# Kernel tuning notes

Hardware: AMD Instinct MI355X
Metric: run time of the kernel (lower is better)

## Reference

```python
import jax, jax.numpy as jnp
import numpy as np

DIM, E, K, H = 1024, 8, 2, 4096

def setup_inputs() -> dict:
    key = jax.random.key(0)
    ks = jax.random.split(key, 5)
    s_in = 1.0 / np.sqrt(DIM)
    s_h = 1.0 / np.sqrt(H)
    return {
        "x": jax.random.normal(ks[0], (4, 2048, DIM), dtype=jnp.float32),
        "Wr": jax.random.normal(ks[1], (DIM, E), dtype=jnp.float32) * s_in,
        "W1": jax.random.normal(ks[2], (E, DIM, H), dtype=jnp.float32) * s_in,
        "b1": jnp.zeros((E, H), dtype=jnp.float32),
        "W2": jax.random.normal(ks[3], (E, H, DIM), dtype=jnp.float32) * s_h,
        "b2": jnp.zeros((E, DIM), dtype=jnp.float32),
    }

def reference(x, Wr, W1, b1, W2, b2):
    batch, seq, dim = x.shape
    x_flat = x.reshape(-1, dim)                      # [T, D]
    logits = x_flat @ Wr                             # [T, E]
    w, ind = jax.lax.top_k(logits, K)                # [T, K]
    w = jax.nn.softmax(w, axis=-1)
    # combine[t, e] = sum_i w[t, i] * (ind[t, i] == e)
    combine = jnp.einsum('tke,tk->te', jax.nn.one_hot(ind, E, dtype=x.dtype), w)  # [T, E]

    def body(acc, params):
        W1e, b1e, W2e, b2e, ce = params
        h = jax.nn.gelu(x_flat @ W1e + b1e, approximate=False)  # exact GELU (torch nn.GELU default)
        y = h @ W2e + b2e                                        # [T, D]
        return acc + ce[:, None] * y, None

    out0 = jnp.zeros_like(x_flat)
    out, _ = jax.lax.scan(body, out0, (W1, b1, W2, b2, combine.T))
    return out.reshape(batch, seq, dim)
```

## Files before the change

### kernel.cpp

```cpp
#include <hip/hip_runtime.h>
#include <hip/hip_bf16.h>

#define TDIM 1024
#define NEXP 8
#define NHID 4096

typedef __hip_bfloat16 bf16;
typedef __attribute__((ext_vector_type(8))) short bf16x8;
typedef __attribute__((ext_vector_type(8))) unsigned short u16x8;
typedef __attribute__((ext_vector_type(4))) float f32x4;

__device__ __forceinline__ void gload_lds16(void* lds, const void* g) {
  __builtin_amdgcn_global_load_lds(
      (const __attribute__((address_space(1))) unsigned int*)g,
      (__attribute__((address_space(3))) unsigned int*)lds, 16, 0, 0);
}

__device__ __forceinline__ unsigned short f2bf_bits(float f) {
  __hip_bfloat16 b = __float2bfloat16(f);
  unsigned short u;
  __builtin_memcpy(&u, &b, 2);
  return u;
}

__device__ __forceinline__ float bf2f(unsigned short u) {
  union { unsigned int i; float f; } c;
  c.i = ((unsigned int)u) << 16;
  return c.f;
}

__device__ __forceinline__ void cvt_quad(const float* __restrict__ src, bf16* __restrict__ dst,
                                         int gid, int ngShift, int rowLen) {
  const int kqg = gid >> ngShift;
  const int ng = gid & ((1 << ngShift) - 1);
  const float* s = src + ((size_t)kqg * 8) * rowLen + ng * 4;
  float4 v[8];
#pragma unroll
  for (int j = 0; j < 8; ++j) v[j] = *reinterpret_cast<const float4*>(s + (size_t)j * rowLen);
  u16x8 o[4];
#pragma unroll
  for (int c = 0; c < 4; ++c)
#pragma unroll
    for (int j = 0; j < 8; ++j) o[c][j] = f2bf_bits((&v[j].x)[c]);
  bf16* d = dst + ((size_t)kqg * rowLen + ng * 4) * 8;
#pragma unroll
  for (int c = 0; c < 4; ++c) *reinterpret_cast<u16x8*>(d + c * 8) = o[c];
}

__global__ __launch_bounds__(256) void prep_kernel(
    const float* __restrict__ W1, bf16* __restrict__ W1C, const float* __restrict__ x,
    bf16* __restrict__ xb, const float* __restrict__ Wr, int* __restrict__ idx,
    float* __restrict__ wtok, int* __restrict__ cnt, int T) {
  __shared__ float xs[4][1024];
  const int pb = blockIdx.x;
  const int tid = threadIdx.x;
  if (pb < 4096) {
    cvt_quad(W1, W1C, pb * 256 + tid, 10, 4096);
  } else {
    const int p = pb - 4096;
    const int wave = p * 4 + (tid >> 6);
    const int lane = tid & 63;
    if (wave >= T) return;
    float* xrow = xs[tid >> 6];
    const float4* xr4 = reinterpret_cast<const float4*>(x + (size_t)wave * TDIM);
    bf16* xbrow = xb + (size_t)wave * TDIM;
#pragma unroll
    for (int i = 0; i < TDIM / 256; ++i) {
      float4 xv = xr4[lane + i * 64];
      ushort4 o;
      o.x = f2bf_bits(xv.x);
      o.y = f2bf_bits(xv.y);
      o.z = f2bf_bits(xv.z);
      o.w = f2bf_bits(xv.w);
      *reinterpret_cast<ushort4*>(xbrow + (lane + i * 64) * 4) = o;
      *reinterpret_cast<float4*>(&xrow[(lane + i * 64) * 4]) = xv;
    }
    float acc[NEXP];
#pragma unroll
    for (int e = 0; e < NEXP; ++e) acc[e] = 0.f;
    const float4* wr4 = reinterpret_cast<const float4*>(Wr);
#pragma unroll
    for (int i = 0; i < TDIM / 64; ++i) {
      float xv = xrow[lane + i * 64];
      float4 wa = wr4[(lane + i * 64) * 2];
      float4 wb = wr4[(lane + i * 64) * 2 + 1];
      acc[0] += xv * wa.x;
      acc[1] += xv * wa.y;
      acc[2] += xv * wa.z;
      acc[3] += xv * wa.w;
      acc[4] += xv * wb.x;
      acc[5] += xv * wb.y;
      acc[6] += xv * wb.z;
      acc[7] += xv * wb.w;
    }
#pragma unroll
    for (int e = 0; e < NEXP; ++e) {
      float v = acc[e];
#pragma unroll
      for (int s = 32; s; s >>= 1) v += __shfl_xor(v, s);
      acc[e] = v;
    }
    if (lane == 0) {
      int e0 = 0;
      float l0 = acc[0];
      for (int e = 1; e < NEXP; ++e)
        if (acc[e] > l0) { l0 = acc[e]; e0 = e; }
      int e1 = -1;
      float l1 = -INFINITY;
      for (int e = 0; e < NEXP; ++e)
        if (e != e0 && acc[e] > l1) { l1 = acc[e]; e1 = e; }
      float z = __expf(l1 - l0);
      idx[wave * 2] = e0;
      idx[wave * 2 + 1] = e1;
      wtok[wave * 2] = 1.f / (1.f + z);
      wtok[wave * 2 + 1] = z / (1.f + z);
      atomicAdd(&cnt[e0], 1);
      atomicAdd(&cnt[e1], 1);
    }
  }
}

__global__ void scan_kernel(const int* __restrict__ cnt, int* __restrict__ offs) {
  if (threadIdx.x == 0 && blockIdx.x == 0) {
    int s = 0;
    for (int e = 0; e < NEXP; ++e) { offs[e] = s; s += cnt[e]; }
  }
}

__global__ void build_perm_kernel(const int* __restrict__ idx, const int* __restrict__ offs,
                                  int* __restrict__ fill, int* __restrict__ perm,
                                  int* __restrict__ islot, int T) {
  int t = blockIdx.x * blockDim.x + threadIdx.x;
  if (t >= T) return;
#pragma unroll
  for (int k = 0; k < 2; ++k) {
    int e = idx[t * 2 + k];
    int p = offs[e] + atomicAdd(&fill[e], 1);
    perm[p] = t;
    islot[t * 2 + k] = p;
  }
}

#define DSR(dst, va, IMM) \
  asm volatile("ds_read_b128 %0, %1 offset:%2" : "=&v"(dst) : "v"(va), "i"(IMM))

template <int KD, int ND, bool GATHER, bool GELU, bool CONV>
__global__ __launch_bounds__(512, 2) void moe_gemm8(
    const bf16* __restrict__ A, const bf16* __restrict__ BC, const float* __restrict__ bias,
    const int* __restrict__ perm, const int* __restrict__ cnt, const int* __restrict__ offs,
    bf16* __restrict__ Dst, int nm, int nn, const float* __restrict__ Wsrc,
    bf16* __restrict__ Wdst) {
  __shared__ short lds[65536];

  const int nwg = NEXP * nm * nn;
  const int bid = blockIdx.x;
  if (CONV && bid >= nwg) {
    const int gid = (bid - nwg) * 512 + threadIdx.x;
    cvt_quad(Wsrc, Wdst, gid, 8, 1024);
    return;
  }
  const int wg = (bid & 7) * (nwg >> 3) + (bid >> 3);
  const int e = wg / (nm * nn);
  const int rem = wg % (nm * nn);
  const int mb = rem / nn, nb = rem % nn;

  const int ce = cnt[e];
  const int m0 = mb * 256;
  if (m0 >= ce) return;
  const int base = offs[e];
  const int n0 = nb * 256;
  const int tid = threadIdx.x;
  const int lane = tid & 63;
  const int wid = tid >> 6;
  const int wm = wid >> 2, wn = wid & 3;
  const int lcol = lane & 15;

  const unsigned ldsb = (unsigned)(size_t)&lds[0];
  const int v4 = lane >> 4;
  const int j7 = lcol & 7;
  const unsigned bk0 = (unsigned)((v4 ^ j7) << 4);
  const unsigned bk1 = (unsigned)(((v4 + 4) ^ j7) << 4);
  const unsigned aBase = ldsb + (unsigned)((wm * 64 + lcol) * 128);
  const unsigned vaA00 = aBase + bk0, vaA01 = aBase + bk1;
  const unsigned vaA10 = aBase + 65536u + bk0, vaA11 = aBase + 65536u + bk1;
  const unsigned bBase = ldsb + 32768u + (unsigned)(v4 * 2048 + (wn * 32 + lcol) * 16);
  const unsigned vaB0 = bBase, vaB1 = bBase + 65536u;

  const bf16* aP[2][2];
  const bf16* bP[2][2];
#pragma unroll
  for (int h = 0; h < 2; ++h)
#pragma unroll
    for (int i = 0; i < 2; ++i) {
      int s = tid + i * 512;
      int srow = s >> 3;
      int ksrc = (s & 7) ^ (srow & 7);
      int grow = m0 + h * 128 + srow;
      if (grow > ce - 1) grow = ce - 1;
      size_t arow = GATHER ? (size_t)perm[base + grow] : (size_t)(base + grow);
      aP[h][i] = A + arow * KD + ksrc * 8;
      int jo = s >> 7, brow = s & 127;
      bP[h][i] = BC + (size_t)e * KD * ND + ((size_t)jo * ND + (n0 + h * 128 + brow)) * 8;
    }

  f32x4 acc[8][4];
#pragma unroll
  for (int m = 0; m < 8; ++m)
#pragma unroll
    for (int n = 0; n < 4; ++n) acc[m][n] = (f32x4){0.f, 0.f, 0.f, 0.f};

  bf16x8 fA[4][2], fB[2][2];

#define STAGE(SBUF, OP, HF, kA, kB)                                                  \
  {                                                                                  \
    char* sd = (char*)lds + (SBUF) * 65536 + (OP) * 32768 + (HF) * 16384 + tid * 16; \
    if (OP) {                                                                        \
      gload_lds16(sd, bP[HF][0] + (kB));                                             \
      gload_lds16(sd + 8192, bP[HF][1] + (kB));                                      \
    } else {                                                                         \
      gload_lds16(sd, aP[HF][0] + (kA));                                             \
      gload_lds16(sd + 8192, aP[HF][1] + (kA));                                      \
    }                                                                                \
  }

#define PHASE(QM, QN, RA, RB, SOP, SHF, SBUF, CBUF, kA, kB, DO_VM)                   \
  {                                                                                  \
    if (RA) {                                                                        \
      DSR(fA[0][0], vaA##CBUF##0, (QM)*16384 + 0);                                   \
      DSR(fA[0][1], vaA##CBUF##1, (QM)*16384 + 0);                                   \
      DSR(fA[1][0], vaA##CBUF##0, (QM)*16384 + 2048);                                \
      DSR(fA[1][1], vaA##CBUF##1, (QM)*16384 + 2048);                                \
      DSR(fA[2][0], vaA##CBUF##0, (QM)*16384 + 4096);                                \
      DSR(fA[2][1], vaA##CBUF##1, (QM)*16384 + 4096);                                \
      DSR(fA[3][0], vaA##CBUF##0, (QM)*16384 + 6144);                                \
      DSR(fA[3][1], vaA##CBUF##1, (QM)*16384 + 6144);                                \
    }                                                                                \
    if (RB) {                                                                        \
      DSR(fB[0][0], vaB##CBUF, (QN)*16384 + 0);                                      \
      DSR(fB[0][1], vaB##CBUF, (QN)*16384 + 8192);                                   \
      DSR(fB[1][0], vaB##CBUF, (QN)*16384 + 256);                                    \
      DSR(fB[1][1], vaB##CBUF, (QN)*16384 + 8192 + 256);                             \
    }                                                                                \
    STAGE(SBUF, SOP, SHF, kA, kB);                                                   \
    if (DO_VM) asm volatile("s_waitcnt vmcnt(4)" ::: "memory");                      \
    __builtin_amdgcn_s_barrier();                                                    \
    asm volatile("s_waitcnt lgkmcnt(0)" ::: "memory");                               \
    __builtin_amdgcn_sched_barrier(0);                                               \
    __builtin_amdgcn_s_setprio(1);                                                   \
    _Pragma("unroll") for (int mm = 0; mm < 4; ++mm)                                 \
        _Pragma("unroll") for (int n2 = 0; n2 < 2; ++n2) {                           \
      acc[(QM) * 4 + mm][(QN) * 2 + n2] = __builtin_amdgcn_mfma_f32_16x16x32_bf16(   \
          fA[mm][0], fB[n2][0], acc[(QM) * 4 + mm][(QN) * 2 + n2], 0, 0, 0);         \
      acc[(QM) * 4 + mm][(QN) * 2 + n2] = __builtin_amdgcn_mfma_f32_16x16x32_bf16(   \
          fA[mm][1], fB[n2][1], acc[(QM) * 4 + mm][(QN) * 2 + n2], 0, 0, 0);         \
    }                                                                                \
    __builtin_amdgcn_s_setprio(0);                                                   \
    __builtin_amdgcn_s_barrier();                                                    \
  }

  STAGE(0, 0, 0, 0, 0);
  STAGE(0, 1, 0, 0, 0);
  STAGE(0, 0, 1, 0, 0);
  STAGE(0, 1, 1, 0, 0);
  asm volatile("s_waitcnt vmcnt(4)" ::: "memory");
  __builtin_amdgcn_s_barrier();

  const int NI = KD / 128;
  for (int itv = 0; itv < NI; ++itv) {
    const int k1 = itv * 128 + 64;
    int k2 = itv * 128 + 128;
    if (k2 >= KD) k2 = 0;
    const int k1B = k1 * ND, k2B = k2 * ND;
    PHASE(0, 0, 1, 1, 0, 0, 1, 0, k1, k1B, 1)
    PHASE(1, 0, 1, 0, 1, 0, 1, 0, k1, k1B, 1)
    PHASE(1, 1, 0, 1, 0, 1, 1, 0, k1, k1B, 0)
    PHASE(0, 1, 1, 0, 1, 1, 1, 0, k1, k1B, 1)
    PHASE(0, 0, 1, 1, 0, 0, 0, 1, k2, k2B, 1)
    PHASE(1, 0, 1, 0, 1, 0, 0, 1, k2, k2B, 1)
    PHASE(1, 1, 0, 1, 0, 1, 0, 1, k2, k2B, 0)
    PHASE(0, 1, 1, 0, 1, 1, 0, 1, k2, k2B, 1)
  }
#undef PHASE
#undef STAGE

  float bv[4];
#pragma unroll
  for (int ni = 0; ni < 4; ++ni)
    bv[ni] = bias[e * ND + n0 + (ni >> 1) * 128 + wn * 32 + (ni & 1) * 16 + lcol];
  const int lr4 = (lane >> 4) * 4;
#pragma unroll
  for (int mi = 0; mi < 8; ++mi) {
    const int rbase = m0 + (mi >> 2) * 128 + wm * 64 + (mi & 3) * 16 + lr4;
#pragma unroll
    for (int r = 0; r < 4; ++r) {
      int grow = rbase + r;
      if (grow < ce) {
        bf16* drow = Dst + (size_t)(base + grow) * ND;
#pragma unroll
        for (int ni = 0; ni < 4; ++ni) {
          int col = n0 + (ni >> 1) * 128 + wn * 32 + (ni & 1) * 16 + lcol;
          float v = acc[mi][ni][r] + bv[ni];
          if (GELU) v = 0.5f * v * (1.0f + erff(v * 0.70710678118654752f));
          drow[col] = __float2bfloat16(v);
        }
      }
    }
  }
}

__global__ void combine_kernel(const bf16* __restrict__ y, const int* __restrict__ islot,
                               const float* __restrict__ wtok, float* __restrict__ out) {
  const int t = blockIdx.x;
  const int d = threadIdx.x * 4;
  const int s0 = islot[t * 2], s1 = islot[t * 2 + 1];
  const float w0 = wtok[t * 2], w1 = wtok[t * 2 + 1];
  ushort4 ya = *reinterpret_cast<const ushort4*>(y + (size_t)s0 * TDIM + d);
  ushort4 yb = *reinterpret_cast<const ushort4*>(y + (size_t)s1 * TDIM + d);
  float4 o;
  o.x = w0 * bf2f(ya.x) + w1 * bf2f(yb.x);
  o.y = w0 * bf2f(ya.y) + w1 * bf2f(yb.y);
  o.z = w0 * bf2f(ya.z) + w1 * bf2f(yb.z);
  o.w = w0 * bf2f(ya.w) + w1 * bf2f(yb.w);
  *reinterpret_cast<float4*>(out + (size_t)t * TDIM + d) = o;
}

extern "C" void kernel_launch(void* const* d_in, const int* in_sizes, int n_in, void* d_out,
                              int out_size, void* d_ws, size_t ws_size, hipStream_t stream) {
  const float* x = (const float*)d_in[0];
  const float* Wr = (const float*)d_in[1];
  const float* W1 = (const float*)d_in[2];
  const float* b1 = (const float*)d_in[3];
  const float* W2 = (const float*)d_in[4];
  const float* b2 = (const float*)d_in[5];
  float* out = (float*)d_out;
  const int T = in_sizes[0] / TDIM;

  size_t off = 0;
  auto alloc = [&](size_t bytes) {
    void* q = (char*)d_ws + off;
    off += (bytes + 255) & ~(size_t)255;
    return q;
  };
  bf16* xb = (bf16*)alloc((size_t)T * TDIM * 2);
  bf16* W1C = (bf16*)alloc((size_t)NEXP * TDIM * NHID * 2);
  bf16* W2C = (bf16*)alloc((size_t)NEXP * TDIM * NHID * 2);
  bf16* h = (bf16*)alloc((size_t)2 * T * NHID * 2);
  int* idx = (int*)alloc((size_t)T * 2 * 4);
  float* wtok = (float*)alloc((size_t)T * 2 * 4);
  int* perm = (int*)alloc((size_t)T * 2 * 4);
  int* islot = (int*)alloc((size_t)T * 2 * 4);
  int* cnt = (int*)alloc(256);
  int* fill = cnt + 8;
  int* offs = cnt + 16;
  bf16* y = W1C;

  hipMemsetAsync(cnt, 0, 64, stream);

  prep_kernel<<<6144, 256, 0, stream>>>(W1, W1C, x, xb, Wr, idx, wtok, cnt, T);
  scan_kernel<<<1, 64, 0, stream>>>(cnt, offs);
  build_perm_kernel<<<(T + 255) / 256, 256, 0, stream>>>(idx, offs, fill, perm, islot, T);

  moe_gemm8<TDIM, NHID, true, true, true><<<NEXP * 32 * 16 + 2048, 512, 0, stream>>>(
      xb, W1C, b1, perm, cnt, offs, h, 32, 16, W2, W2C);
  moe_gemm8<NHID, TDIM, false, false, false><<<NEXP * 32 * 4, 512, 0, stream>>>(
      h, W2C, b2, perm, cnt, offs, y, 32, 4, nullptr, nullptr);

  combine_kernel<<<T, 256, 0, stream>>>(y, islot, wtok, out);
}
```

Measured before the change: 783.8 us.

## Restructure GEMM pipeline to whole-tile staging and move W2 conversion to prep

The GEMM main loop now issues all four global-to-LDS loads for the next K tile at once, waits with vmcnt(8), and computes four MFMA quads on the current buffer between only two barriers per tile. Previously each quad was interleaved with one staged load and its own pair of barriers. This cuts barrier count, at the cost of less fine-grained overlap between loads and compute. The W2 fp32-to-bf16 conversion also moves from extra blocks in the first GEMM launch into the prep kernel, so the first GEMM runs only compute blocks.

```diff
diff --git a/kernel.cpp b/kernel.cpp
--- a/kernel.cpp
+++ b/kernel.cpp
@@ -48,16 +48,19 @@
 }
 
 __global__ __launch_bounds__(256) void prep_kernel(
-    const float* __restrict__ W1, bf16* __restrict__ W1C, const float* __restrict__ x,
-    bf16* __restrict__ xb, const float* __restrict__ Wr, int* __restrict__ idx,
-    float* __restrict__ wtok, int* __restrict__ cnt, int T) {
+    const float* __restrict__ W1, bf16* __restrict__ W1C, const float* __restrict__ W2,
+    bf16* __restrict__ W2C, const float* __restrict__ x, bf16* __restrict__ xb,
+    const float* __restrict__ Wr, int* __restrict__ idx, float* __restrict__ wtok,
+    int* __restrict__ cnt, int T) {
   __shared__ float xs[4][1024];
   const int pb = blockIdx.x;
   const int tid = threadIdx.x;
   if (pb < 4096) {
     cvt_quad(W1, W1C, pb * 256 + tid, 10, 4096);
+  } else if (pb < 8192) {
+    cvt_quad(W2, W2C, (pb - 4096) * 256 + tid, 8, 1024);
   } else {
-    const int p = pb - 4096;
+    const int p = pb - 8192;
     const int wave = p * 4 + (tid >> 6);
     const int lane = tid & 63;
     if (wave >= T) return;
@@ -144,21 +147,15 @@
 #define DSR(dst, va, IMM) \
   asm volatile("ds_read_b128 %0, %1 offset:%2" : "=&v"(dst) : "v"(va), "i"(IMM))
 
-template <int KD, int ND, bool GATHER, bool GELU, bool CONV>
-__global__ __launch_bounds__(512, 2) void moe_gemm8(
+template <int KD, int ND, bool GATHER, bool GELU>
+__global__ __launch_bounds__(512, 2) void moe_gemm2p(
     const bf16* __restrict__ A, const bf16* __restrict__ BC, const float* __restrict__ bias,
     const int* __restrict__ perm, const int* __restrict__ cnt, const int* __restrict__ offs,
-    bf16* __restrict__ Dst, int nm, int nn, const float* __restrict__ Wsrc,
-    bf16* __restrict__ Wdst) {
+    bf16* __restrict__ Dst, int nm, int nn) {
   __shared__ short lds[65536];
 
   const int nwg = NEXP * nm * nn;
   const int bid = blockIdx.x;
-  if (CONV && bid >= nwg) {
-    const int gid = (bid - nwg) * 512 + threadIdx.x;
-    cvt_quad(Wsrc, Wdst, gid, 8, 1024);
-    return;
-  }
   const int wg = (bid & 7) * (nwg >> 3) + (bid >> 3);
   const int e = wg / (nm * nn);
   const int rem = wg % (nm * nn);
@@ -223,7 +220,7 @@
     }                                                                                \
   }
 
-#define PHASE(QM, QN, RA, RB, SOP, SHF, SBUF, CBUF, kA, kB, DO_VM)                   \
+#define QUAD(QM, QN, RA, RB, CBUF)                                                   \
   {                                                                                  \
     if (RA) {                                                                        \
       DSR(fA[0][0], vaA##CBUF##0, (QM)*16384 + 0);                                   \
@@ -241,9 +238,6 @@
       DSR(fB[1][0], vaB##CBUF, (QN)*16384 + 256);                                    \
       DSR(fB[1][1], vaB##CBUF, (QN)*16384 + 8192 + 256);                             \
     }                                                                                \
-    STAGE(SBUF, SOP, SHF, kA, kB);                                                   \
-    if (DO_VM) asm volatile("s_waitcnt vmcnt(4)" ::: "memory");                      \
-    __builtin_amdgcn_s_barrier();                                                    \
     asm volatile("s_waitcnt lgkmcnt(0)" ::: "memory");                               \
     __builtin_amdgcn_sched_barrier(0);                                               \
     __builtin_amdgcn_s_setprio(1);                                                   \
@@ -255,6 +249,20 @@
           fA[mm][1], fB[n2][1], acc[(QM) * 4 + mm][(QN) * 2 + n2], 0, 0, 0);         \
     }                                                                                \
     __builtin_amdgcn_s_setprio(0);                                                   \
+  }
+
+#define TILE(CB, SB, kA, kB)                                                         \
+  {                                                                                  \
+    STAGE(SB, 0, 0, kA, kB);                                                         \
+    STAGE(SB, 1, 0, kA, kB);                                                         \
+    STAGE(SB, 0, 1, kA, kB);                                                         \
+    STAGE(SB, 1, 1, kA, kB);                                                         \
+    asm volatile("s_waitcnt vmcnt(8)" ::: "memory");                                 \
+    __builtin_amdgcn_s_barrier();                                                    \
+    QUAD(0, 0, 1, 1, CB)                                                             \
+    QUAD(1, 0, 1, 0, CB)                                                             \
+    QUAD(1, 1, 0, 1, CB)                                                             \
+    QUAD(0, 1, 1, 0, CB)                                                             \
     __builtin_amdgcn_s_barrier();                                                    \
   }
 
@@ -262,8 +270,6 @@
   STAGE(0, 1, 0, 0, 0);
   STAGE(0, 0, 1, 0, 0);
   STAGE(0, 1, 1, 0, 0);
-  asm volatile("s_waitcnt vmcnt(4)" ::: "memory");
-  __builtin_amdgcn_s_barrier();
 
   const int NI = KD / 128;
   for (int itv = 0; itv < NI; ++itv) {
@@ -271,16 +277,11 @@
     int k2 = itv * 128 + 128;
     if (k2 >= KD) k2 = 0;
     const int k1B = k1 * ND, k2B = k2 * ND;
-    PHASE(0, 0, 1, 1, 0, 0, 1, 0, k1, k1B, 1)
-    PHASE(1, 0, 1, 0, 1, 0, 1, 0, k1, k1B, 1)
-    PHASE(1, 1, 0, 1, 0, 1, 1, 0, k1, k1B, 0)
-    PHASE(0, 1, 1, 0, 1, 1, 1, 0, k1, k1B, 1)
-    PHASE(0, 0, 1, 1, 0, 0, 0, 1, k2, k2B, 1)
-    PHASE(1, 0, 1, 0, 1, 0, 0, 1, k2, k2B, 1)
-    PHASE(1, 1, 0, 1, 0, 1, 0, 1, k2, k2B, 0)
-    PHASE(0, 1, 1, 0, 1, 1, 0, 1, k2, k2B, 1)
-  }
-#undef PHASE
+    TILE(0, 1, k1, k1B)
+    TILE(1, 0, k2, k2B)
+  }
+#undef TILE
+#undef QUAD
 #undef STAGE
 
   float bv[4];
@@ -356,14 +357,14 @@
 
   hipMemsetAsync(cnt, 0, 64, stream);
 
-  prep_kernel<<<6144, 256, 0, stream>>>(W1, W1C, x, xb, Wr, idx, wtok, cnt, T);
+  prep_kernel<<<10240, 256, 0, stream>>>(W1, W1C, W2, W2C, x, xb, Wr, idx, wtok, cnt, T);
   scan_kernel<<<1, 64, 0, stream>>>(cnt, offs);
   build_perm_kernel<<<(T + 255) / 256, 256, 0, stream>>>(idx, offs, fill, perm, islot, T);
 
-  moe_gemm8<TDIM, NHID, true, true, true><<<NEXP * 32 * 16 + 2048, 512, 0, stream>>>(
-      xb, W1C, b1, perm, cnt, offs, h, 32, 16, W2, W2C);
-  moe_gemm8<NHID, TDIM, false, false, false><<<NEXP * 32 * 4, 512, 0, stream>>>(
-      h, W2C, b2, perm, cnt, offs, y, 32, 4, nullptr, nullptr);
+  moe_gemm2p<TDIM, NHID, true, true><<<NEXP * 32 * 16, 512, 0, stream>>>(
+      xb, W1C, b1, perm, cnt, offs, h, 32, 16);
+  moe_gemm2p<NHID, TDIM, false, false><<<NEXP * 32 * 4, 512, 0, stream>>>(
+      h, W2C, b2, perm, cnt, offs, y, 32, 4);
 
   combine_kernel<<<T, 256, 0, stream>>>(y, islot, wtok, out);
 }
```

Result: slower. 835.7 us (+6.6%).
